# Optimization experiments

Measured on AMD Instinct MI355X. Metric: run time of the kernel, lower is better.

Reference implementation:

```python
import math
import jax, jax.numpy as jnp
import numpy as np

B, S, HID = 1, 2048, 2048
H, D = 32, 64            # heads, head_dim = HID // H
THETA = 10000.0
EPS = 1e-6
LAYER_IDX = 12
LAM_INIT = 0.8 - 0.6 * math.exp(-0.3 * LAYER_IDX)  # lambda_init_fn(layer_idx)
SCALE = 1.0 / math.sqrt(D)


def _rope_cos_sin(seq_len, dim):
    inv_freq = 1.0 / (THETA ** (np.arange(0, dim, 2, dtype=np.float64) / dim))
    freqs = np.outer(np.arange(seq_len, dtype=np.float64), inv_freq)
    emb = np.concatenate([freqs, freqs], axis=-1)  # [S, D] (llama duplicates freqs)
    return jnp.asarray(np.cos(emb), jnp.float32), jnp.asarray(np.sin(emb), jnp.float32)


def _rotate_half(x):
    return jnp.concatenate([-x[..., D // 2:], x[..., : D // 2]], axis=-1)


def _apply_rope(x, cos, sin):
    # x: [B, H, S, D]; cos/sin: [S, D] broadcast over B, H
    return x * cos + _rotate_half(x) * sin


def setup_inputs() -> dict:
    key = jax.random.key(0)
    ks = jax.random.split(key, 10)
    return {
        "hidden_states": jax.random.normal(ks[0], (B, S, HID), jnp.float32),
        "Wq": jax.random.normal(ks[1], (2 * HID, HID), jnp.float32) * 0.02,
        "Wk": jax.random.normal(ks[2], (2 * HID, HID), jnp.float32) * 0.02,
        "Wv": jax.random.normal(ks[3], (HID, HID), jnp.float32) * 0.02,
        "Wo": jax.random.normal(ks[4], (HID, HID), jnp.float32) * 0.02,
        "lambda_q1": jax.random.normal(ks[5], (D,), jnp.float32) * 0.1,
        "lambda_k1": jax.random.normal(ks[6], (D,), jnp.float32) * 0.1,
        "lambda_q2": jax.random.normal(ks[7], (D,), jnp.float32) * 0.1,
        "lambda_k2": jax.random.normal(ks[8], (D,), jnp.float32) * 0.1,
        "subln_w": jnp.ones((D,), jnp.float32),
    }


def reference(hidden_states, Wq, Wk, Wv, Wo,
              lambda_q1, lambda_k1, lambda_q2, lambda_k2, subln_w):
    # Projections (nn.Linear, no bias): x @ W.T
    q = hidden_states @ Wq.T                       # [B, S, 2*HID]
    k = hidden_states @ Wk.T                       # [B, S, 2*HID]
    v = hidden_states @ Wv.T                       # [B, S, HID]

    def to_heads(t):  # [B, S, H*D] -> [B, H, S, D]
        return t.reshape(B, S, H, D).transpose(0, 2, 1, 3)

    q1, q2 = jnp.split(q, 2, axis=-1)
    k1, k2 = jnp.split(k, 2, axis=-1)
    q1, q2, k1, k2, v = map(to_heads, (q1, q2, k1, k2, v))

    cos, sin = _rope_cos_sin(S, D)
    q1, k1 = _apply_rope(q1, cos, sin), _apply_rope(k1, cos, sin)
    q2, k2 = _apply_rope(q2, cos, sin), _apply_rope(k2, cos, sin)

    # Causal additive mask [S, S]
    causal = jnp.tril(jnp.ones((S, S), bool))
    neg_inf = jnp.finfo(jnp.float32).min
    mask = jnp.where(causal, 0.0, neg_inf)

    s1 = jnp.einsum("bhqd,bhkd->bhqk", q1, k1) * SCALE + mask
    s2 = jnp.einsum("bhqd,bhkd->bhqk", q2, k2) * SCALE + mask

    lam = (jnp.exp(jnp.sum(lambda_q1 * lambda_k1))
           - jnp.exp(jnp.sum(lambda_q2 * lambda_k2)) + LAM_INIT)

    attn_w = jax.nn.softmax(s1, axis=-1) - lam * jax.nn.softmax(s2, axis=-1)
    attn = jnp.einsum("bhqk,bhkd->bhqd", attn_w, v)  # [B, H, S, D]

    # Head-wise RMSNorm (LlamaRMSNorm over value_head_dim)
    var = jnp.mean(jnp.square(attn), axis=-1, keepdims=True)
    attn = attn * jax.lax.rsqrt(var + EPS) * subln_w
    attn = attn * (1.0 - LAM_INIT)

    out = attn.transpose(0, 2, 1, 3).reshape(B, S, HID) @ Wo.T
    return out
```

## Files before the change

### kernel.cpp

```cpp
#include <hip/hip_runtime.h>


typedef __bf16 bf16;
typedef __bf16 bf16x4 __attribute__((ext_vector_type(4)));
typedef __bf16 bf16x8 __attribute__((ext_vector_type(8)));
typedef float  f32x4  __attribute__((ext_vector_type(4)));
typedef unsigned int u32;
typedef u32 u32x2 __attribute__((ext_vector_type(2)));
typedef u32 u32x4 __attribute__((ext_vector_type(4)));

#define MFMA(a, b, c) __builtin_amdgcn_mfma_f32_16x16x32_bf16((a), (b), (c), 0, 0, 0)

#define S_LEN   2048
#define HID_DIM 2048
#define NHEAD   32
#define HD      64
#define QKV_N   10240
#define LAM_INIT 0.7836057665316245f
#define ONE_MINUS_LAM_INIT 0.21639423346837553f
#define QSCALE  0.18033688011112042f
#define RMS_EPS 1e-6f
#define L2T     0.4152410118609203f

__device__ __forceinline__ void gld16(const void* g, void* l) {
    __builtin_amdgcn_global_load_lds(
        (const __attribute__((address_space(1))) void*)g,
        (__attribute__((address_space(3))) void*)l, 16, 0, 0);
}

__device__ __forceinline__ void pa_build(u32 x, u32 y, int quad, u32& wlo, u32& whi) {
#if __has_builtin(__builtin_amdgcn_permlane32_swap) && __has_builtin(__builtin_amdgcn_permlane16_swap)
    u32x2 s = __builtin_amdgcn_permlane32_swap(x, y, false, false);
    u32x2 t = __builtin_amdgcn_permlane16_swap(s.x, s.y, false, false);
    wlo = t.x;
    whi = t.y;
#else
    const u32 x16 = (u32)__shfl_xor((int)x, 16, 64);
    const u32 x32 = (u32)__shfl_xor((int)x, 32, 64);
    const u32 x48 = (u32)__shfl_xor((int)x, 48, 64);
    const u32 y16 = (u32)__shfl_xor((int)y, 16, 64);
    const u32 y32 = (u32)__shfl_xor((int)y, 32, 64);
    const u32 y48 = (u32)__shfl_xor((int)y, 48, 64);
    wlo = (quad == 0) ? x   : (quad == 1) ? x48 : (quad == 2) ? y32 : y16;
    whi = (quad == 0) ? x16 : (quad == 1) ? x32 : (quad == 2) ? y48 : y;
#endif
}

__global__ void cvt_all(const float* __restrict__ hs, const float* __restrict__ Wq,
                        const float* __restrict__ Wk, const float* __restrict__ Wv,
                        const float* __restrict__ Wo,
                        const float* __restrict__ lq1, const float* __restrict__ lk1,
                        const float* __restrict__ lq2, const float* __restrict__ lk2,
                        bf16* __restrict__ hsb, bf16* __restrict__ Wb,
                        bf16* __restrict__ Wob, float* __restrict__ lam_out) {
    const int bid = blockIdx.x;
    if (bid >= 14336) {
        const int t = threadIdx.x;
        if (t < 64) {
            float a = lq1[t] * lk1[t];
            float b = lq2[t] * lk2[t];
            #pragma unroll
            for (int off = 32; off > 0; off >>= 1) {
                a += __shfl_xor(a, off, 64);
                b += __shfl_xor(b, off, 64);
            }
            if (t == 0) lam_out[0] = expf(a) - expf(b) + LAM_INIT;
        }
        return;
    }
    const float* src; bf16* dst; int off;
    if      (bid <  2048) { src = hs; dst = hsb;            off = bid;         }
    else if (bid <  6144) { src = Wq; dst = Wb;             off = bid - 2048;  }
    else if (bid < 10240) { src = Wk; dst = Wb +  8388608;  off = bid - 6144;  }
    else if (bid < 12288) { src = Wv; dst = Wb + 16777216;  off = bid - 10240; }
    else                  { src = Wo; dst = Wob;            off = bid - 12288; }
    const int i = off * 2048 + threadIdx.x * 8;
    float4 a = *(const float4*)(src + i);
    float4 b = *(const float4*)(src + i + 4);
    bf16x8 o = { (bf16)a.x, (bf16)a.y, (bf16)a.z, (bf16)a.w,
                 (bf16)b.x, (bf16)b.y, (bf16)b.z, (bf16)b.w };
    *(bf16x8*)(dst + i) = o;
}

__global__ __launch_bounds__(256, 3)
void qkv_rope_gemm(const bf16* __restrict__ A, const bf16* __restrict__ B,
                   bf16* __restrict__ Q1, bf16* __restrict__ Q2,
                   bf16* __restrict__ K1, bf16* __restrict__ K2,
                   bf16* __restrict__ Vt) {
    __shared__ __align__(16) bf16 As[128 * 64];
    __shared__ __align__(16) bf16 Bs[128 * 64];
    const int tid  = threadIdx.x;
    const int wave = tid >> 6, lane = tid & 63;
    const int wm = wave >> 1, wn = wave & 1;
    const int l = lane & 15, quad = lane >> 4;
    const int m0 = blockIdx.y * 128, n0 = blockIdx.x * 128;

    f32x4 acc[4][4];
    #pragma unroll
    for (int i = 0; i < 4; ++i)
        #pragma unroll
        for (int j = 0; j < 4; ++j) acc[i][j] = (f32x4){0.f, 0.f, 0.f, 0.f};

    const int rr  = tid >> 3;
    const int csw = ((tid & 7) ^ (rr & 7)) * 8;
    const bf16* Ag = A + (size_t)(m0 + rr) * HID_DIM + csw;
    const bf16* Bg = B + (size_t)(n0 + rr) * HID_DIM + csw;

    for (int kt = 0; kt < HID_DIM; kt += 64) {
        __syncthreads();
        #pragma unroll
        for (int j = 0; j < 4; ++j) {
            gld16(Ag + (size_t)(32 * j) * HID_DIM + kt, As + j * 2048 + tid * 8);
            gld16(Bg + (size_t)(32 * j) * HID_DIM + kt, Bs + j * 2048 + tid * 8);
        }
        __syncthreads();

        #pragma unroll
        for (int ks = 0; ks < 2; ++ks) {
            const int co = (((ks << 2) | quad) ^ (l & 7)) << 3;
            bf16x8 hf[4], wf[4];
            #pragma unroll
            for (int hi = 0; hi < 4; ++hi)
                hf[hi] = *(const bf16x8*)(As + (wm * 64 + hi * 16 + l) * 64 + co);
            #pragma unroll
            for (int wi = 0; wi < 4; ++wi)
                wf[wi] = *(const bf16x8*)(Bs + (wn * 64 + wi * 16 + l) * 64 + co);
            #pragma unroll
            for (int wi = 0; wi < 4; ++wi)
                #pragma unroll
                for (int hi = 0; hi < 4; ++hi)
                    acc[wi][hi] = MFMA(wf[wi], hf[hi], acc[wi][hi]);
        }
    }

    const int c = n0 + wn * 64;
    const int sbase = m0 + wm * 64;
    bf16* dst; int off; float scale = 1.0f; bool isv = false;
    if      (c < 2048) { dst = Q1; off = c;        scale = QSCALE; }
    else if (c < 4096) { dst = Q2; off = c - 2048; scale = QSCALE; }
    else if (c < 6144) { dst = K1; off = c - 4096; }
    else if (c < 8192) { dst = K2; off = c - 6144; }
    else               { isv = true; off = c - 8192; }
    const int h = off >> 6;

    if (!isv) {
        float invf[2][4];
        #pragma unroll
        for (int p = 0; p < 2; ++p)
            #pragma unroll
            for (int r = 0; r < 4; ++r)
                invf[p][r] = exp2f(-(float)(p * 16 + quad * 4 + r) * L2T);

        #pragma unroll
        for (int hi = 0; hi < 4; ++hi) {
            const float s = (float)(sbase + hi * 16 + l);
            float cs[2][4], sn[2][4];
            #pragma unroll
            for (int p = 0; p < 2; ++p)
                #pragma unroll
                for (int r = 0; r < 4; ++r) {
                    const float ang = s * invf[p][r];
                    cs[p][r] = __cosf(ang);
                    sn[p][r] = __sinf(ang);
                }
            bf16* rowp = dst + ((size_t)h * S_LEN + sbase + hi * 16 + l) * HD + quad * 4;
            #pragma unroll
            for (int wi = 0; wi < 4; ++wi) {
                const int p = wi & 1;
                const float sign = (wi < 2) ? -1.0f : 1.0f;
                bf16x4 o;
                #pragma unroll
                for (int r = 0; r < 4; ++r)
                    o[r] = (bf16)((acc[wi][hi][r] * cs[p][r] +
                                   sign * acc[wi ^ 2][hi][r] * sn[p][r]) * scale);
                *(bf16x4*)(rowp + wi * 16) = o;
            }
        }
    } else {
        #pragma unroll
        for (int wi = 0; wi < 4; ++wi)
            #pragma unroll
            for (int r = 0; r < 4; ++r) {
                bf16* vrow = Vt + ((size_t)h * HD + wi * 16 + quad * 4 + r) * S_LEN + sbase;
                #pragma unroll
                for (int hi = 0; hi < 4; ++hi)
                    vrow[hi * 16 + l] = (bf16)acc[wi][hi][r];
            }
    }
}

__global__ __launch_bounds__(256, 3)
void gemm_bt_splitk(const bf16* __restrict__ A, const bf16* __restrict__ B,
                    float* __restrict__ Cout, int M, int N, int K_total, int K_part) {
    __shared__ __align__(16) bf16 As[128 * 64];
    __shared__ __align__(16) bf16 Bs[128 * 64];
    const int tid  = threadIdx.x;
    const int wave = tid >> 6, lane = tid & 63;
    const int wm = wave >> 1, wn = wave & 1;
    const int l = lane & 15, quad = lane >> 4;
    const int m0 = blockIdx.y * 128, n0 = blockIdx.x * 128;
    const int kz = blockIdx.z * K_part;

    f32x4 acc[4][4];
    #pragma unroll
    for (int i = 0; i < 4; ++i)
        #pragma unroll
        for (int j = 0; j < 4; ++j) acc[i][j] = (f32x4){0.f, 0.f, 0.f, 0.f};

    const int rr  = tid >> 3;
    const int csw = ((tid & 7) ^ (rr & 7)) * 8;
    const bf16* Ag = A + (size_t)(m0 + rr) * K_total + kz + csw;
    const bf16* Bg = B + (size_t)(n0 + rr) * K_total + kz + csw;

    for (int kt = 0; kt < K_part; kt += 64) {
        __syncthreads();
        #pragma unroll
        for (int j = 0; j < 4; ++j) {
            gld16(Ag + (size_t)(32 * j) * K_total + kt, As + j * 2048 + tid * 8);
            gld16(Bg + (size_t)(32 * j) * K_total + kt, Bs + j * 2048 + tid * 8);
        }
        __syncthreads();

        #pragma unroll
        for (int ks = 0; ks < 2; ++ks) {
            const int co = (((ks << 2) | quad) ^ (l & 7)) << 3;
            bf16x8 af[4], bfr[4];
            #pragma unroll
            for (int mi = 0; mi < 4; ++mi)
                af[mi] = *(const bf16x8*)(As + (wm * 64 + mi * 16 + l) * 64 + co);
            #pragma unroll
            for (int ni = 0; ni < 4; ++ni)
                bfr[ni] = *(const bf16x8*)(Bs + (wn * 64 + ni * 16 + l) * 64 + co);
            #pragma unroll
            for (int mi = 0; mi < 4; ++mi)
                #pragma unroll
                for (int ni = 0; ni < 4; ++ni)
                    acc[mi][ni] = MFMA(af[mi], bfr[ni], acc[mi][ni]);
        }
    }

    float* Pf = Cout + (size_t)blockIdx.z * M * N;
    #pragma unroll
    for (int mi = 0; mi < 4; ++mi)
        #pragma unroll
        for (int ni = 0; ni < 4; ++ni)
            #pragma unroll
            for (int r = 0; r < 4; ++r) {
                const int row = m0 + wm * 64 + mi * 16 + quad * 4 + r;
                const int col = n0 + wn * 64 + ni * 16 + l;
                Pf[(size_t)row * N + col] = acc[mi][ni][r];
            }
}

__global__ void reduce_add(const float* __restrict__ p, float* __restrict__ out, int n) {
    const int i = (blockIdx.x * 256 + threadIdx.x) * 4;
    float4 a = *(const float4*)(p + i);
    float4 b = *(const float4*)(p + n + i);
    float4 o = { a.x + b.x, a.y + b.y, a.z + b.z, a.w + b.w };
    *(float4*)(out + i) = o;
}

__global__ __launch_bounds__(512, 2)
void diff_attn(const bf16* __restrict__ Q1, const bf16* __restrict__ K1,
               const bf16* __restrict__ Q2, const bf16* __restrict__ K2,
               const bf16* __restrict__ Vt, const float* __restrict__ lam_p,
               const float* __restrict__ subln_w, bf16* __restrict__ attn_out) {
    const int bid  = blockIdx.x;
    const int h    = bid & 31;
    const int pp   = bid >> 5;
    const int tid  = threadIdx.x;
    const int wave = tid >> 6, lane = tid & 63;
    const int qhalf = wave >> 2, sid = (wave >> 1) & 1, ks = wave & 1;
    const int l = lane & 15, quad = lane >> 4;

    __shared__ __align__(16) char smem[49152];

    const bf16* K1g = K1 + (size_t)h * S_LEN * HD;
    const bf16* K2g = K2 + (size_t)h * S_LEN * HD;
    const bf16* Vtg = Vt + (size_t)h * HD * S_LEN;
    const bf16* Qv  = (sid ? Q2 : Q1) + (size_t)h * S_LEN * HD;

    const int rr  = tid >> 3;
    const int csw = ((tid & 7) ^ (rr & 7)) * 8;
    const int sw8 = l & 7;

    auto stage = [&](int kv, int bufb) {
        gld16(K1g + (size_t)(kv + rr) * HD + csw,  (bf16*)(smem + bufb)         + tid * 8);
        gld16(K2g + (size_t)(kv + rr) * HD + csw,  (bf16*)(smem + bufb + 8192)  + tid * 8);
        gld16(Vtg + (size_t)rr * S_LEN + kv + csw, (bf16*)(smem + bufb + 16384) + tid * 8);
    };

    for (int it = 0; it < 2; ++it) {
        const int qb = it ? pp : (15 - pp);
        const int q0 = qb * 128;
        const bf16* Qh = Qv + (size_t)(q0 + qhalf * 64) * HD;

        bf16x8 qf[4][2];
        #pragma unroll
        for (int g = 0; g < 4; ++g)
            #pragma unroll
            for (int dh = 0; dh < 2; ++dh)
                qf[g][dh] = *(const bf16x8*)(Qh + (g * 16 + l) * HD + dh * 32 + quad * 8);

        f32x4 O[4][4];
        #pragma unroll
        for (int g = 0; g < 4; ++g)
            #pragma unroll
            for (int nd = 0; nd < 4; ++nd)
                O[g][nd] = (f32x4){0.f, 0.f, 0.f, 0.f};
        float csum[4] = {0.f, 0.f, 0.f, 0.f};

        const int T  = 2 * qb + 2;
        const int tq = 2 * qb + qhalf;

        stage(0, 0);
        asm volatile("s_waitcnt vmcnt(0)" ::: "memory");
        __builtin_amdgcn_s_barrier();

        for (int t = 0; t < T; ++t) {
            const int bb = (t & 1) * 24576;
            if (t + 1 < T) stage((t + 1) * 64, 24576 - bb);

            if (t <= tq) {
                const bool diag = (t == tq);
                const bf16* Ksm = (const bf16*)(smem + bb + (sid ? 8192 : 0));
                const bf16* Vts = (const bf16*)(smem + bb + 16384);

                bf16x8 ka[2][2];
                #pragma unroll
                for (int mk = 0; mk < 2; ++mk) {
                    const int krow = ((2 * ks + mk) * 16 + l) * 64;
                    ka[mk][0] = *(const bf16x8*)(Ksm + krow + ((quad ^ sw8) << 3));
                    ka[mk][1] = *(const bf16x8*)(Ksm + krow + (((4 + quad) ^ sw8) << 3));
                }
                bf16x8 vb[4];
                #pragma unroll
                for (int nd = 0; nd < 4; ++nd)
                    vb[nd] = *(const bf16x8*)(Vts + (nd * 16 + l) * 64 +
                                              ((((ks << 2) + quad) ^ sw8) << 3));

                __builtin_amdgcn_s_setprio(1);
                #pragma unroll
                for (int g = 0; g < 4; ++g) {
                    f32x4 c[2];
                    #pragma unroll
                    for (int mk = 0; mk < 2; ++mk) {
                        c[mk] = (f32x4){0.f, 0.f, 0.f, 0.f};
                        c[mk] = MFMA(ka[mk][0], qf[g][0], c[mk]);
                        c[mk] = MFMA(ka[mk][1], qf[g][1], c[mk]);
                    }
                    u32 dw[2][2];
                    float lsum = 0.f;
                    #pragma unroll
                    for (int mk = 0; mk < 2; ++mk) {
                        float p[4];
                        #pragma unroll
                        for (int r = 0; r < 4; ++r) {
                            p[r] = __builtin_amdgcn_exp2f(c[mk][r]);
                            if (diag && ((2 * ks + mk) * 16 + quad * 4 + r > g * 16 + l))
                                p[r] = 0.f;
                            lsum += p[r];
                        }
                        asm("v_cvt_pk_bf16_f32 %0, %1, %2" : "=v"(dw[mk][0]) : "v"(p[0]), "v"(p[1]));
                        asm("v_cvt_pk_bf16_f32 %0, %1, %2" : "=v"(dw[mk][1]) : "v"(p[2]), "v"(p[3]));
                    }
                    csum[g] += lsum;

                    u32 w0, w1, w2, w3;
                    pa_build(dw[0][0], dw[1][0], quad, w0, w2);
                    pa_build(dw[0][1], dw[1][1], quad, w1, w3);
                    u32x4 wv = {w0, w1, w2, w3};
                    bf16x8 pa;
                    __builtin_memcpy(&pa, &wv, 16);

                    #pragma unroll
                    for (int nd = 0; nd < 4; ++nd)
                        O[g][nd] = MFMA(pa, vb[nd], O[g][nd]);
                }
                __builtin_amdgcn_s_setprio(0);
            }

            asm volatile("s_waitcnt vmcnt(0)" ::: "memory");
            __builtin_amdgcn_s_barrier();
        }

        __syncthreads();
        #pragma unroll
        for (int round = 0; round < 2; ++round) {
            float* dO = (float*)(smem + sid * 17408);
            float* dC = (float*)(smem + 34816 + sid * 1024);
            if (qhalf == round && ks == 1) {
                #pragma unroll
                for (int g = 0; g < 4; ++g)
                    #pragma unroll
                    for (int nd = 0; nd < 4; ++nd)
                        *(f32x4*)(dO + lane * 68 + (g * 4 + nd) * 4) = O[g][nd];
                #pragma unroll
                for (int g = 0; g < 4; ++g) dC[g * 64 + lane] = csum[g];
            }
            __syncthreads();
            if (qhalf == round && ks == 0) {
                #pragma unroll
                for (int g = 0; g < 4; ++g) {
                    #pragma unroll
                    for (int nd = 0; nd < 4; ++nd)
                        O[g][nd] += *(const f32x4*)(dO + lane * 68 + (g * 4 + nd) * 4);
                    csum[g] += dC[g * 64 + lane];
                }
            }
            __syncthreads();
        }

        #pragma unroll
        for (int g = 0; g < 4; ++g) {
            csum[g] += __shfl_xor(csum[g], 16, 64);
            csum[g] += __shfl_xor(csum[g], 32, 64);
        }

        float* epi = (float*)smem;

        if (sid == 1 && ks == 0) {
            const float lam = lam_p[0];
            #pragma unroll
            for (int mi = 0; mi < 4; ++mi)
                #pragma unroll
                for (int r = 0; r < 4; ++r) {
                    const float inv = lam / __shfl(csum[mi], quad * 4 + r, 64);
                    const int row = qhalf * 64 + mi * 16 + quad * 4 + r;
                    #pragma unroll
                    for (int ni = 0; ni < 4; ++ni)
                        epi[row * 65 + ni * 16 + l] = O[mi][ni][r] * inv;
                }
        }
        __syncthreads();

        if (sid == 0 && ks == 0) {
            float sw[4];
            #pragma unroll
            for (int ni = 0; ni < 4; ++ni) sw[ni] = subln_w[ni * 16 + l];

            #pragma unroll
            for (int mi = 0; mi < 4; ++mi) {
                float inv1[4];
                #pragma unroll
                for (int r = 0; r < 4; ++r)
                    inv1[r] = 1.0f / __shfl(csum[mi], quad * 4 + r, 64);

                float v[4][4]; float ssq[4] = {0.f, 0.f, 0.f, 0.f};
                #pragma unroll
                for (int ni = 0; ni < 4; ++ni)
                    #pragma unroll
                    for (int r = 0; r < 4; ++r) {
                        const int row = qhalf * 64 + mi * 16 + quad * 4 + r;
                        const float x = O[mi][ni][r] * inv1[r] - epi[row * 65 + ni * 16 + l];
                        v[ni][r] = x;
                        ssq[r] += x * x;
                    }
                #pragma unroll
                for (int r = 0; r < 4; ++r) {
                    float s = ssq[r];
                    s += __shfl_xor(s, 1, 64);
                    s += __shfl_xor(s, 2, 64);
                    s += __shfl_xor(s, 4, 64);
                    s += __shfl_xor(s, 8, 64);
                    ssq[r] = rsqrtf(s * (1.0f / 64.0f) + RMS_EPS) * ONE_MINUS_LAM_INIT;
                }
                #pragma unroll
                for (int ni = 0; ni < 4; ++ni)
                    #pragma unroll
                    for (int r = 0; r < 4; ++r) {
                        const int row = q0 + qhalf * 64 + mi * 16 + quad * 4 + r;
                        attn_out[(size_t)row * HID_DIM + h * 64 + ni * 16 + l] =
                            (bf16)(v[ni][r] * ssq[r] * sw[ni]);
                    }
            }
        }
        __syncthreads();
    }
}

extern "C" void kernel_launch(void* const* d_in, const int* in_sizes, int n_in,
                              void* d_out, int out_size, void* d_ws, size_t ws_size,
                              hipStream_t stream) {
    const float* hs  = (const float*)d_in[0];
    const float* Wq  = (const float*)d_in[1];
    const float* Wk  = (const float*)d_in[2];
    const float* Wv  = (const float*)d_in[3];
    const float* Wo  = (const float*)d_in[4];
    const float* lq1 = (const float*)d_in[5];
    const float* lk1 = (const float*)d_in[6];
    const float* lq2 = (const float*)d_in[7];
    const float* lk2 = (const float*)d_in[8];
    const float* slw = (const float*)d_in[9];

    if (ws_size < 151000000u) return;

    char* ws = (char*)d_ws;
    bf16*  hsb  = (bf16*)(ws);
    bf16*  Wb   = (bf16*)(ws + 8388608);
    bf16*  Wob  = (bf16*)(ws + 50331648);
    float* part = (float*)(ws + 58720256);
    bf16*  Q1b  = (bf16*)(ws + 100663296);
    bf16*  K1b  = (bf16*)(ws + 109051904);
    bf16*  Q2b  = (bf16*)(ws + 117440512);
    bf16*  K2b  = (bf16*)(ws + 125829120);
    bf16*  Vtb  = (bf16*)(ws + 134217728);
    bf16*  abuf = (bf16*)(ws + 142606336);
    float* lamp = (float*)(ws + 150994944);

    cvt_all<<<14337, 256, 0, stream>>>(hs, Wq, Wk, Wv, Wo, lq1, lk1, lq2, lk2,
                                       hsb, Wb, Wob, lamp);

    qkv_rope_gemm<<<dim3(QKV_N / 128, S_LEN / 128), 256, 0, stream>>>(
        hsb, Wb, Q1b, Q2b, K1b, K2b, Vtb);

    diff_attn<<<256, 512, 0, stream>>>(Q1b, K1b, Q2b, K2b, Vtb, lamp, slw, abuf);

    gemm_bt_splitk<<<dim3(HID_DIM / 128, S_LEN / 128, 2), 256, 0, stream>>>(
        abuf, Wob, part, S_LEN, HID_DIM, HID_DIM, HID_DIM / 2);
    reduce_add<<<4096, 256, 0, stream>>>(part, (float*)d_out, S_LEN * HID_DIM);
}
```

Before: 343.8 us.

## Stage 128-key tiles per barrier in diff_attn and remap split-K GEMM blocks across XCDs

The attention kernel now stages 128 keys per iteration (two 64-key subtiles) into a doubled 96KB LDS double buffer. This halves the number of barrier/waitcnt synchronisations per query block. Separately, the split-K GEMM remaps linear block ids so that blocks on the same XCD share contiguous M/N tiles, which should improve L2 reuse. The larger LDS footprint may cut attention occupancy from 2 blocks per CU, and the GEMM remap hardcodes a 16x16 grid.

```diff
diff --git a/kernel.cpp b/kernel.cpp
--- a/kernel.cpp
+++ b/kernel.cpp
@@ -198,14 +198,17 @@
     const int wave = tid >> 6, lane = tid & 63;
     const int wm = wave >> 1, wn = wave & 1;
     const int l = lane & 15, quad = lane >> 4;
-    const int m0 = blockIdx.y * 128, n0 = blockIdx.x * 128;
+    const int lin = blockIdx.y * 16 + blockIdx.x;
+    const int xcd = lin & 7, j = lin >> 3;
+    const int m0 = (((xcd >> 1) << 2) + (j & 3)) * 128;
+    const int n0 = (((xcd & 1) << 3) + (j >> 2)) * 128;
     const int kz = blockIdx.z * K_part;
 
     f32x4 acc[4][4];
     #pragma unroll
     for (int i = 0; i < 4; ++i)
         #pragma unroll
-        for (int j = 0; j < 4; ++j) acc[i][j] = (f32x4){0.f, 0.f, 0.f, 0.f};
+        for (int j2 = 0; j2 < 4; ++j2) acc[i][j2] = (f32x4){0.f, 0.f, 0.f, 0.f};
 
     const int rr  = tid >> 3;
     const int csw = ((tid & 7) ^ (rr & 7)) * 8;
@@ -215,9 +218,9 @@
     for (int kt = 0; kt < K_part; kt += 64) {
         __syncthreads();
         #pragma unroll
-        for (int j = 0; j < 4; ++j) {
-            gld16(Ag + (size_t)(32 * j) * K_total + kt, As + j * 2048 + tid * 8);
-            gld16(Bg + (size_t)(32 * j) * K_total + kt, Bs + j * 2048 + tid * 8);
+        for (int jj = 0; jj < 4; ++jj) {
+            gld16(Ag + (size_t)(32 * jj) * K_total + kt, As + jj * 2048 + tid * 8);
+            gld16(Bg + (size_t)(32 * jj) * K_total + kt, Bs + jj * 2048 + tid * 8);
         }
         __syncthreads();
 
@@ -273,7 +276,7 @@
     const int qhalf = wave >> 2, sid = (wave >> 1) & 1, ks = wave & 1;
     const int l = lane & 15, quad = lane >> 4;
 
-    __shared__ __align__(16) char smem[49152];
+    __shared__ __align__(16) char smem[98304];
 
     const bf16* K1g = K1 + (size_t)h * S_LEN * HD;
     const bf16* K2g = K2 + (size_t)h * S_LEN * HD;
@@ -285,9 +288,15 @@
     const int sw8 = l & 7;
 
     auto stage = [&](int kv, int bufb) {
-        gld16(K1g + (size_t)(kv + rr) * HD + csw,  (bf16*)(smem + bufb)         + tid * 8);
-        gld16(K2g + (size_t)(kv + rr) * HD + csw,  (bf16*)(smem + bufb + 8192)  + tid * 8);
-        gld16(Vtg + (size_t)rr * S_LEN + kv + csw, (bf16*)(smem + bufb + 16384) + tid * 8);
+        #pragma unroll
+        for (int s = 0; s < 2; ++s) {
+            gld16(K1g + (size_t)(kv + s * 64 + rr) * HD + csw,
+                  (bf16*)(smem + bufb)         + s * 4096 + tid * 8);
+            gld16(K2g + (size_t)(kv + s * 64 + rr) * HD + csw,
+                  (bf16*)(smem + bufb + 16384) + s * 4096 + tid * 8);
+            gld16(Vtg + (size_t)rr * S_LEN + kv + s * 64 + csw,
+                  (bf16*)(smem + bufb + 32768) + s * 4096 + tid * 8);
+        }
     };
 
     for (int it = 0; it < 2; ++it) {
@@ -310,74 +319,79 @@
                 O[g][nd] = (f32x4){0.f, 0.f, 0.f, 0.f};
         float csum[4] = {0.f, 0.f, 0.f, 0.f};
 
-        const int T  = 2 * qb + 2;
+        const int nt = qb + 1;
         const int tq = 2 * qb + qhalf;
 
         stage(0, 0);
         asm volatile("s_waitcnt vmcnt(0)" ::: "memory");
         __builtin_amdgcn_s_barrier();
 
-        for (int t = 0; t < T; ++t) {
-            const int bb = (t & 1) * 24576;
-            if (t + 1 < T) stage((t + 1) * 64, 24576 - bb);
-
-            if (t <= tq) {
-                const bool diag = (t == tq);
-                const bf16* Ksm = (const bf16*)(smem + bb + (sid ? 8192 : 0));
-                const bf16* Vts = (const bf16*)(smem + bb + 16384);
-
-                bf16x8 ka[2][2];
-                #pragma unroll
-                for (int mk = 0; mk < 2; ++mk) {
-                    const int krow = ((2 * ks + mk) * 16 + l) * 64;
-                    ka[mk][0] = *(const bf16x8*)(Ksm + krow + ((quad ^ sw8) << 3));
-                    ka[mk][1] = *(const bf16x8*)(Ksm + krow + (((4 + quad) ^ sw8) << 3));
+        for (int tt = 0; tt < nt; ++tt) {
+            const int bb = (tt & 1) * 49152;
+            if (tt + 1 < nt) stage((tt + 1) * 128, 49152 - bb);
+
+            #pragma unroll
+            for (int sub = 0; sub < 2; ++sub) {
+                const int t64 = 2 * tt + sub;
+                if (t64 <= tq) {
+                    const bool diag = (t64 == tq);
+                    const bf16* Ksm = (const bf16*)(smem + bb + (sid ? 16384 : 0))
+                                      + sub * 4096;
+                    const bf16* Vts = (const bf16*)(smem + bb + 32768) + sub * 4096;
+
+                    bf16x8 ka[2][2];
+                    #pragma unroll
+                    for (int mk = 0; mk < 2; ++mk) {
+                        const int krow = ((2 * ks + mk) * 16 + l) * 64;
+                        ka[mk][0] = *(const bf16x8*)(Ksm + krow + ((quad ^ sw8) << 3));
+                        ka[mk][1] = *(const bf16x8*)(Ksm + krow + (((4 + quad) ^ sw8) << 3));
+                    }
+                    bf16x8 vb[4];
+                    #pragma unroll
+                    for (int nd = 0; nd < 4; ++nd)
+                        vb[nd] = *(const bf16x8*)(Vts + (nd * 16 + l) * 64 +
+                                                  ((((ks << 2) + quad) ^ sw8) << 3));
+
+                    __builtin_amdgcn_s_setprio(1);
+                    #pragma unroll
+                    for (int g = 0; g < 4; ++g) {
+                        f32x4 c[2];
+                        #pragma unroll
+                        for (int mk = 0; mk < 2; ++mk) {
+                            c[mk] = (f32x4){0.f, 0.f, 0.f, 0.f};
+                            c[mk] = MFMA(ka[mk][0], qf[g][0], c[mk]);
+                            c[mk] = MFMA(ka[mk][1], qf[g][1], c[mk]);
+                        }
+                        u32 dw[2][2];
+                        float lsum = 0.f;
+                        #pragma unroll
+                        for (int mk = 0; mk < 2; ++mk) {
+                            float p[4];
+                            #pragma unroll
+                            for (int r = 0; r < 4; ++r) {
+                                p[r] = __builtin_amdgcn_exp2f(c[mk][r]);
+                                if (diag && ((2 * ks + mk) * 16 + quad * 4 + r > g * 16 + l))
+                                    p[r] = 0.f;
+                                lsum += p[r];
+                            }
+                            asm("v_cvt_pk_bf16_f32 %0, %1, %2" : "=v"(dw[mk][0]) : "v"(p[0]), "v"(p[1]));
+                            asm("v_cvt_pk_bf16_f32 %0, %1, %2" : "=v"(dw[mk][1]) : "v"(p[2]), "v"(p[3]));
+                        }
+                        csum[g] += lsum;
+
+                        u32 w0, w1, w2, w3;
+                        pa_build(dw[0][0], dw[1][0], quad, w0, w2);
+                        pa_build(dw[0][1], dw[1][1], quad, w1, w3);
+                        u32x4 wv = {w0, w1, w2, w3};
+                        bf16x8 pa;
+                        __builtin_memcpy(&pa, &wv, 16);
+
+                        #pragma unroll
+                        for (int nd = 0; nd < 4; ++nd)
+                            O[g][nd] = MFMA(pa, vb[nd], O[g][nd]);
+                    }
+                    __builtin_amdgcn_s_setprio(0);
                 }
-                bf16x8 vb[4];
-                #pragma unroll
-                for (int nd = 0; nd < 4; ++nd)
-                    vb[nd] = *(const bf16x8*)(Vts + (nd * 16 + l) * 64 +
-                                              ((((ks << 2) + quad) ^ sw8) << 3));
-
-                __builtin_amdgcn_s_setprio(1);
-                #pragma unroll
-                for (int g = 0; g < 4; ++g) {
-                    f32x4 c[2];
-                    #pragma unroll
-                    for (int mk = 0; mk < 2; ++mk) {
-                        c[mk] = (f32x4){0.f, 0.f, 0.f, 0.f};
-                        c[mk] = MFMA(ka[mk][0], qf[g][0], c[mk]);
-                        c[mk] = MFMA(ka[mk][1], qf[g][1], c[mk]);
-                    }
-                    u32 dw[2][2];
-                    float lsum = 0.f;
-                    #pragma unroll
-                    for (int mk = 0; mk < 2; ++mk) {
-                        float p[4];
-                        #pragma unroll
-                        for (int r = 0; r < 4; ++r) {
-                            p[r] = __builtin_amdgcn_exp2f(c[mk][r]);
-                            if (diag && ((2 * ks + mk) * 16 + quad * 4 + r > g * 16 + l))
-                                p[r] = 0.f;
-                            lsum += p[r];
-                        }
-                        asm("v_cvt_pk_bf16_f32 %0, %1, %2" : "=v"(dw[mk][0]) : "v"(p[0]), "v"(p[1]));
-                        asm("v_cvt_pk_bf16_f32 %0, %1, %2" : "=v"(dw[mk][1]) : "v"(p[2]), "v"(p[3]));
-                    }
-                    csum[g] += lsum;
-
-                    u32 w0, w1, w2, w3;
-                    pa_build(dw[0][0], dw[1][0], quad, w0, w2);
-                    pa_build(dw[0][1], dw[1][1], quad, w1, w3);
-                    u32x4 wv = {w0, w1, w2, w3};
-                    bf16x8 pa;
-                    __builtin_memcpy(&pa, &wv, 16);
-
-                    #pragma unroll
-                    for (int nd = 0; nd < 4; ++nd)
-                        O[g][nd] = MFMA(pa, vb[nd], O[g][nd]);
-                }
-                __builtin_amdgcn_s_setprio(0);
             }
 
             asm volatile("s_waitcnt vmcnt(0)" ::: "memory");
```

Result: no change. 343.2 us (-0.2%).
